# Optimization experiments

Measured on AMD Instinct MI355X. Metric: run time of the kernel, lower is better.

The kernel has to match this reference:

```python
import jax, jax.numpy as jnp
import numpy as np

INPUT_DIM = 512
OUTPUT_DIM = 512
GRID_SIZE = 16
INPUT_MIN = -1.0
INPUT_RANGE = 2.0


def setup_inputs() -> dict:
    key = jax.random.key(0)
    k_x, k_mix = jax.random.split(key)
    x = jax.random.normal(k_x, (65536, INPUT_DIM), dtype=jnp.float32)
    # per-dim spline tables: bases init zeros, slopes init 0.1 (as in torch)
    bases = jnp.zeros((INPUT_DIM, GRID_SIZE), dtype=jnp.float32)
    slopes = jnp.full((INPUT_DIM, GRID_SIZE), 0.1, dtype=jnp.float32)
    mix = jax.random.normal(k_mix, (OUTPUT_DIM, INPUT_DIM), dtype=jnp.float32) * 0.01
    bias = jnp.zeros((OUTPUT_DIM,), dtype=jnp.float32)
    return {"x": x, "bases": bases, "slopes": slopes, "mix": mix, "bias": bias}


def reference(x, bases, slopes, mix, bias):
    # x: [B, D]; bases/slopes: [D, G]; mix: [O, D]; bias: [O]
    B, D = x.shape
    G = bases.shape[1]
    x_norm = jnp.clip((x - INPUT_MIN) / INPUT_RANGE, 0.0, 1.0 - 1e-6)
    idx = jnp.clip((x_norm * G).astype(jnp.int32), 0, G - 1)        # [B, D]
    x_local = x_norm * G - idx.astype(x.dtype)                       # fractional position in cell
    # gather per-dim table entries: flatten [D, G] and index with d*G + idx
    flat_idx = jnp.arange(D, dtype=jnp.int32)[None, :] * G + idx    # [B, D]
    base = bases.reshape(-1)[flat_idx]                               # [B, D]
    slope = slopes.reshape(-1)[flat_idx]                             # [B, D]
    spline_out = base + slope * x_local                              # [B, D]
    y = jnp.einsum('bd,od->bo', spline_out, mix) + bias              # [B, O]
    return y
```

## Files before the change

### kernel.cpp

```cpp
#include <hip/hip_runtime.h>


#define DIMK 512
#define DIMN 512

typedef unsigned short u16;
typedef unsigned int u32;
typedef __attribute__((ext_vector_type(8))) __bf16 bf16x8;
typedef __attribute__((ext_vector_type(4))) float f32x4;

__device__ __forceinline__ u32 bf16rne(float f) {
    u32 u = __float_as_uint(f);
    return (u + 0x7fffu + ((u >> 16) & 1u)) >> 16;
}

__global__ void prep_kernel(const float* __restrict__ mix,
                            u16* __restrict__ mixb) {
    int t = blockIdx.x * 256 + threadIdx.x;
    float4 v = reinterpret_cast<const float4*>(mix)[t];
    ushort4 o;
    o.x = (u16)bf16rne(v.x);
    o.y = (u16)bf16rne(v.y);
    o.z = (u16)bf16rne(v.z);
    o.w = (u16)bf16rne(v.w);
    reinterpret_cast<ushort4*>(mixb)[t] = o;
}

__device__ __forceinline__ int tab_word(int dim, int g) {
    return dim * 16 + (g ^ (((dim >> 3) & 3) << 2));
}

__global__ __launch_bounds__(512, 4) void kan_kernel(
    const float* __restrict__ x, const float* __restrict__ bases,
    const float* __restrict__ slopes, const u16* __restrict__ mixb,
    const float* __restrict__ bias, float* __restrict__ y) {
    __shared__ u32 s_tab[DIMK * 16];
    __shared__ __align__(16) u16 sA[2][128 * 32];
    __shared__ __align__(16) u16 sB[2][256 * 32];

    const int tid = threadIdx.x;
    const int lane = tid & 63;
    const int wid = tid >> 6;
    const int quad = lane >> 4;
    const int l15 = lane & 15;
    const int wave_m = wid >> 1;
    const int wave_n = wid & 1;
    const int swz = (blockIdx.x & 7) * 128 + (blockIdx.x >> 3);
    const int m0 = (swz >> 1) * 128;
    const int n0 = (swz & 1) * 256;

#pragma unroll
    for (int k = 0; k < 16; k++) {
        int i = tid + k * 512;
        u32 p = bf16rne(bases[i]) | (bf16rne(slopes[i]) << 16);
        s_tab[tab_word(i >> 4, i & 15)] = p;
    }

    const int ar = tid >> 2;
    const int akg = tid & 3;
    const int awchunk = (ar << 2) | (akg ^ ((ar >> 1) & 3));
    const float4* xrow =
        reinterpret_cast<const float4*>(x + (size_t)(m0 + ar) * DIMK) + akg * 2;

    f32x4 acc[2][8];
#pragma unroll
    for (int i = 0; i < 2; i++)
#pragma unroll
        for (int j = 0; j < 8; j++) acc[i][j] = (f32x4){0.f, 0.f, 0.f, 0.f};

    auto stage_a = [&](u16* sAb, float4 a, float4 b, int kt) {
        float xs[8] = {a.x, a.y, a.z, a.w, b.x, b.y, b.z, b.w};
        const int dbase = kt * 32 + akg * 8;
        u32 h[8];
#pragma unroll
        for (int j = 0; j < 8; j++) {
            float xn = fminf(fmaxf((xs[j] + 1.0f) * 0.5f, 0.0f), 0.999999f);
            float tt = xn * 16.0f;
            int idx = (int)tt;
            u32 p = s_tab[tab_word(dbase + j, idx)];
            float base = __uint_as_float(p << 16);
            float slope = __uint_as_float(p & 0xffff0000u);
            float sp = fmaf(slope, tt - (float)idx, base);
            h[j] = bf16rne(sp);
        }
        int4 pk = make_int4((int)(h[0] | (h[1] << 16)), (int)(h[2] | (h[3] << 16)),
                            (int)(h[4] | (h[5] << 16)), (int)(h[6] | (h[7] << 16)));
        *reinterpret_cast<int4*>(&sAb[awchunk * 8]) = pk;
    };
    auto stage_b = [&](u16* sBb, int kt) {
#pragma unroll
        for (int i = 0; i < 2; i++) {
            int grp = wid * 2 + i;
            int n = grp * 16 + (lane >> 2);
            int c = (lane & 3) ^ ((n >> 1) & 3);
            const u16* gsrc = mixb + (size_t)(n0 + n) * DIMK + kt * 32 + c * 8;
            __builtin_amdgcn_global_load_lds(
                (const __attribute__((address_space(1))) void*)gsrc,
                (__attribute__((address_space(3))) void*)(&sBb[grp * 512]),
                16, 0, 0);
        }
    };

    float4 p0 = xrow[0], p1 = xrow[1];
    __syncthreads();
    stage_a(&sA[0][0], p0, p1, 0);
    stage_b(&sB[0][0], 0);
    float4 xs0a = xrow[8], xs0b = xrow[9];
    __syncthreads();

    for (int kt = 0; kt < 16; ++kt) {
        const int p = kt & 1;
        const int q = p ^ 1;

        if (kt < 15) stage_b(&sB[q][0], kt + 1);

        float4 xna = xs0a, xnb = xs0b;
        if (kt < 14) {
            xna = xrow[(kt + 2) * 8];
            xnb = xrow[(kt + 2) * 8 + 1];
        }

        if (kt < 15) stage_a(&sA[q][0], xs0a, xs0b, kt + 1);

        const u16* sAc = &sA[p][0];
        const u16* sBc = &sB[p][0];
        bf16x8 afrag[2];
#pragma unroll
        for (int fm = 0; fm < 2; fm++) {
            int m_l = wave_m * 32 + fm * 16 + l15;
            int ci = (m_l << 2) | (quad ^ ((m_l >> 1) & 3));
            afrag[fm] = *reinterpret_cast<const bf16x8*>(&sAc[ci * 8]);
        }
#pragma unroll
        for (int fn = 0; fn < 8; fn++) {
            int n_l = wave_n * 128 + fn * 16 + l15;
            int ci = (n_l << 2) | (quad ^ ((n_l >> 1) & 3));
            bf16x8 bfrag = *reinterpret_cast<const bf16x8*>(&sBc[ci * 8]);
#pragma unroll
            for (int fm = 0; fm < 2; fm++)
                acc[fm][fn] = __builtin_amdgcn_mfma_f32_16x16x32_bf16(
                    afrag[fm], bfrag, acc[fm][fn], 0, 0, 0);
        }

        if (kt < 15) __syncthreads();
        xs0a = xna; xs0b = xnb;
    }

#pragma unroll
    for (int fn = 0; fn < 8; fn++) {
        int o = n0 + wave_n * 128 + fn * 16 + l15;
        float bv = bias[o];
#pragma unroll
        for (int fm = 0; fm < 2; fm++) {
            int row = m0 + wave_m * 32 + fm * 16 + quad * 4;
            float* yp = y + (size_t)row * DIMN + o;
#pragma unroll
            for (int j = 0; j < 4; j++)
                yp[(size_t)j * DIMN] = acc[fm][fn][j] + bv;
        }
    }
}

extern "C" void kernel_launch(void* const* d_in, const int* in_sizes, int n_in,
                              void* d_out, int out_size, void* d_ws, size_t ws_size,
                              hipStream_t stream) {
    const float* x = (const float*)d_in[0];
    const float* bases = (const float*)d_in[1];
    const float* slopes = (const float*)d_in[2];
    const float* mix = (const float*)d_in[3];
    const float* bias = (const float*)d_in[4];
    float* y = (float*)d_out;

    u16* mixb = (u16*)d_ws;

    hipLaunchKernelGGL(prep_kernel, dim3(256), dim3(256), 0, stream, mix, mixb);
    hipLaunchKernelGGL(kan_kernel, dim3(1024), dim3(512), 0, stream,
                       x, bases, slopes, mixb, bias, y);
}
```

Measured before the change: 271.2 us.

## Relayout spline table g-major and hand-schedule waits with partial vmcnt barriers

The spline lookup table in LDS becomes g-major with an XOR swizzle of the dim index, which spreads lanes of a wave across banks differently during the gather. The main loop replaces __syncthreads with explicit sched_barriers plus an s_waitcnt vmcnt(2) and s_barrier. This lets the prefetched x loads for the next-next tile stay in flight across the barrier instead of being drained. MFMA sections are raised to priority 1 via s_setprio. The hand-written waitcnt depends on a specific ordering of memory ops, which is fragile if the compiler reorders them.

```diff
diff --git a/kernel.cpp b/kernel.cpp
--- a/kernel.cpp
+++ b/kernel.cpp
@@ -26,15 +26,11 @@
     reinterpret_cast<ushort4*>(mixb)[t] = o;
 }
 
-__device__ __forceinline__ int tab_word(int dim, int g) {
-    return dim * 16 + (g ^ (((dim >> 3) & 3) << 2));
-}
-
 __global__ __launch_bounds__(512, 4) void kan_kernel(
     const float* __restrict__ x, const float* __restrict__ bases,
     const float* __restrict__ slopes, const u16* __restrict__ mixb,
     const float* __restrict__ bias, float* __restrict__ y) {
-    __shared__ u32 s_tab[DIMK * 16];
+    __shared__ u32 s_tab[16 * DIMK];
     __shared__ __align__(16) u16 sA[2][128 * 32];
     __shared__ __align__(16) u16 sB[2][256 * 32];
 
@@ -52,8 +48,9 @@
 #pragma unroll
     for (int k = 0; k < 16; k++) {
         int i = tid + k * 512;
+        int dim = i >> 4, g = i & 15;
         u32 p = bf16rne(bases[i]) | (bf16rne(slopes[i]) << 16);
-        s_tab[tab_word(i >> 4, i & 15)] = p;
+        s_tab[g * DIMK + (dim ^ g)] = p;
     }
 
     const int ar = tid >> 2;
@@ -77,7 +74,7 @@
             float xn = fminf(fmaxf((xs[j] + 1.0f) * 0.5f, 0.0f), 0.999999f);
             float tt = xn * 16.0f;
             int idx = (int)tt;
-            u32 p = s_tab[tab_word(dbase + j, idx)];
+            u32 p = s_tab[idx * DIMK + ((dbase + j) ^ idx)];
             float base = __uint_as_float(p << 16);
             float slope = __uint_as_float(p & 0xffff0000u);
             float sp = fmaf(slope, tt - (float)idx, base);
@@ -103,24 +100,31 @@
 
     float4 p0 = xrow[0], p1 = xrow[1];
     __syncthreads();
+    stage_b(&sB[0][0], 0);
+    __builtin_amdgcn_sched_barrier(0);
+    float4 xs0a = xrow[8], xs0b = xrow[9];
+    __builtin_amdgcn_sched_barrier(0);
     stage_a(&sA[0][0], p0, p1, 0);
-    stage_b(&sB[0][0], 0);
-    float4 xs0a = xrow[8], xs0b = xrow[9];
-    __syncthreads();
+    __builtin_amdgcn_sched_barrier(0);
+    asm volatile("s_waitcnt vmcnt(2) lgkmcnt(0)" ::: "memory");
+    __builtin_amdgcn_sched_barrier(0);
+    __builtin_amdgcn_s_barrier();
 
     for (int kt = 0; kt < 16; ++kt) {
         const int p = kt & 1;
         const int q = p ^ 1;
-
-        if (kt < 15) stage_b(&sB[q][0], kt + 1);
+        const bool do_stage = (kt < 15);
 
         float4 xna = xs0a, xnb = xs0b;
-        if (kt < 14) {
-            xna = xrow[(kt + 2) * 8];
-            xnb = xrow[(kt + 2) * 8 + 1];
+        if (do_stage) {
+            stage_b(&sB[q][0], kt + 1);
+            __builtin_amdgcn_sched_barrier(0);
+            const int ktn = ((kt + 2) & 15) * 8;
+            xna = xrow[ktn];
+            xnb = xrow[ktn + 1];
+            __builtin_amdgcn_sched_barrier(0);
+            stage_a(&sA[q][0], xs0a, xs0b, kt + 1);
         }
-
-        if (kt < 15) stage_a(&sA[q][0], xs0a, xs0b, kt + 1);
 
         const u16* sAc = &sA[p][0];
         const u16* sBc = &sB[p][0];
@@ -131,6 +135,7 @@
             int ci = (m_l << 2) | (quad ^ ((m_l >> 1) & 3));
             afrag[fm] = *reinterpret_cast<const bf16x8*>(&sAc[ci * 8]);
         }
+        __builtin_amdgcn_s_setprio(1);
 #pragma unroll
         for (int fn = 0; fn < 8; fn++) {
             int n_l = wave_n * 128 + fn * 16 + l15;
@@ -141,9 +146,16 @@
                 acc[fm][fn] = __builtin_amdgcn_mfma_f32_16x16x32_bf16(
                     afrag[fm], bfrag, acc[fm][fn], 0, 0, 0);
         }
+        __builtin_amdgcn_s_setprio(0);
 
-        if (kt < 15) __syncthreads();
-        xs0a = xna; xs0b = xnb;
+        if (do_stage) {
+            __builtin_amdgcn_sched_barrier(0);
+            asm volatile("s_waitcnt vmcnt(2) lgkmcnt(0)" ::: "memory");
+            __builtin_amdgcn_sched_barrier(0);
+            __builtin_amdgcn_s_barrier();
+        }
+        xs0a = xna;
+        xs0b = xnb;
     }
 
 #pragma unroll
```

After: 266.9 us. About the same (-1.6%).
